# Kernel tuning notes

Measured on AMD Instinct MI355X. Metric: run time of the kernel, lower is better.

Reference implementation:

```python
import jax, jax.numpy as jnp
import numpy as np


def setup_inputs() -> dict:
    key = jax.random.key(0)
    ks = jax.random.split(key, 8)
    N, NL, C, E, P3, P2, P1 = 2048, 16, 128, 10, 23, 4, 1
    return {
        "x": jax.random.normal(ks[0], (N, NL, C), dtype=jnp.float32),
        "atom_types": jax.random.randint(ks[1], (N,), 0, E),
        "U3": jax.random.normal(ks[2], (NL, NL, NL, P3), dtype=jnp.float32),
        "U2": jax.random.normal(ks[3], (NL, NL, P2), dtype=jnp.float32),
        "U1": jax.random.normal(ks[4], (NL, P1), dtype=jnp.float32),
        "W3": jax.random.normal(ks[5], (E, P3, C), dtype=jnp.float32),
        "W2": jax.random.normal(ks[6], (E, P2, C), dtype=jnp.float32),
        "W1": jax.random.normal(ks[7], (E, P1, C), dtype=jnp.float32),
    }


def reference(x, atom_types, U3, U2, U1, W3, W2, W1):
    # MACE symmetric contraction, correlation order 3, per-atom-type weights.
    # x: [N, nl, C]; atom_types: [N]; U3: [nl,nl,nl,P3]; W3: [E,P3,C]; etc.
    w3 = W3[atom_types]  # [N, P3, C]
    w2 = W2[atom_types]  # [N, P2, C]
    w1 = W1[atom_types]  # [N, P1, C]
    # Correlation-3 term: c3[n,a,b,c] = sum_{i,k} U3[a,b,i,k] * w3[n,k,c] * x[n,i,c]
    xw = jnp.einsum('nkc,nic->nkic', w3, x)        # [N, P3, nl, C]
    c3 = jnp.einsum('abik,nkic->nabc', U3, xw)     # [N, nl, nl, C]
    # Add correlation-2 term, contract one nl index with x.
    c2 = c3 + jnp.einsum('abk,nkc->nabc', U2, w2)  # [N, nl, nl, C]
    c1 = jnp.einsum('nabc,nbc->nac', c2, x)        # [N, nl, C]
    # Add correlation-1 term, contract last nl index with x.
    c1 = c1 + jnp.einsum('ak,nkc->nac', U1, w1)    # [N, nl, C]
    out = jnp.einsum('nac,nac->nc', c1, x)         # [N, C]
    return out
```

## Files before the change

kernel.cpp:

```cpp
#include <hip/hip_runtime.h>


constexpr int NL = 16;
constexpr int CC = 128;
constexpr int EE = 10;
constexpr int P3 = 23;
constexpr int P2 = 4;
constexpr int NTRI = 816;
constexpr int NPAIR = 136;
constexpr int GG = 2;

constexpr int pairsBefore(int a) {
    int s = 0;
    for (int x = 0; x < a; x++) s += NL - x;
    return s;
}
constexpr int trisBefore(int a) {
    int s = 0;
    for (int x = 0; x < a; x++) s += (NL - x) * (NL - x + 1) / 2;
    return s;
}
static_assert(trisBefore(2) % 4 == 0 && trisBefore(4) % 4 == 0 && trisBefore(8) % 4 == 0, "");

__global__ void k_symU(const float* __restrict__ U3, const float* __restrict__ U2,
                       float* __restrict__ U3s, float* __restrict__ U2s,
                       float* __restrict__ out, int out_n, int* __restrict__ counts) {
    int gtid = blockIdx.x * blockDim.x + threadIdx.x;
    int nthreads = gridDim.x * blockDim.x;
    if (gtid < 16) counts[gtid] = 0;
    for (int idx = gtid; idx < out_n; idx += nthreads) out[idx] = 0.f;
    int idx = gtid;
    if (idx < NTRI * P3) {
        int tri = idx / P3, k = idx % P3;
        int rem = tri, a = 0;
        while (rem >= (NL - a) * (NL - a + 1) / 2) { rem -= (NL - a) * (NL - a + 1) / 2; a++; }
        int b = a;
        while (rem >= NL - b) { rem -= NL - b; b++; }
        int i = b + rem;
        auto u = [&](int p, int q, int r) { return U3[((p * NL + q) * NL + r) * P3 + k]; };
        float s = u(a,b,i) + u(a,i,b) + u(b,a,i) + u(b,i,a) + u(i,a,b) + u(i,b,a);
        int m = (a == b && b == i) ? 6 : ((a == b || b == i) ? 2 : 1);
        U3s[idx] = s / (float)m;
    } else if (idx < NTRI * P3 + NPAIR * P2) {
        int j = idx - NTRI * P3;
        int pr = j / P2, k = j % P2;
        int rem = pr, a = 0;
        while (rem >= NL - a) { rem -= NL - a; a++; }
        int b = a + rem;
        float s = U2[(a * NL + b) * P2 + k];
        if (a != b) s += U2[(b * NL + a) * P2 + k];
        U2s[pr * P2 + k] = s;
    }
}

__global__ __launch_bounds__(256) void k_buildA(const float* __restrict__ U3s,
                                                const float* __restrict__ U2s,
                                                const float* __restrict__ U1,
                                                const float* __restrict__ W3,
                                                const float* __restrict__ W2,
                                                const float* __restrict__ W1,
                                                float* __restrict__ A3, float* __restrict__ A2,
                                                float* __restrict__ A1) {
    int blk = blockIdx.x;
    int tid = threadIdx.x;
    if (blk < EE * 8) {
        int t = blk / 8, chunk = blk % 8;
        __shared__ float W3s[P3 * CC];
        __shared__ float U3c[102 * P3];
        for (int idx = tid; idx < P3 * CC; idx += 256) W3s[idx] = W3[t * P3 * CC + idx];
        for (int idx = tid; idx < 102 * P3; idx += 256) U3c[idx] = U3s[chunk * 102 * P3 + idx];
        __syncthreads();
        int c = tid & 127, h = tid >> 7;
        for (int j = 0; j < 51; j++) {
            int tsub = h * 51 + j;
            int tri = chunk * 102 + tsub;
            float s = 0.f;
            #pragma unroll
            for (int k = 0; k < P3; k++) s += U3c[tsub * P3 + k] * W3s[k * CC + c];
            A3[(((size_t)t * (NTRI / 4) + (tri >> 2)) * CC + c) * 4 + (tri & 3)] = s;
        }
    } else {
        int t = blk - EE * 8;
        __shared__ float W2s[P2 * CC];
        __shared__ float U2c[NPAIR * P2];
        for (int idx = tid; idx < P2 * CC; idx += 256) W2s[idx] = W2[t * P2 * CC + idx];
        for (int idx = tid; idx < NPAIR * P2; idx += 256) U2c[idx] = U2s[idx];
        __syncthreads();
        int c = tid & 127, h = tid >> 7;
        for (int j = 0; j < NPAIR / 2; j++) {
            int pr = h * (NPAIR / 2) + j;
            float s = 0.f;
            #pragma unroll
            for (int k = 0; k < P2; k++) s += U2c[pr * P2 + k] * W2s[k * CC + c];
            A2[((size_t)t * NPAIR + pr) * CC + c] = s;
        }
        if (h == 0)
            for (int a = 0; a < NL; a++)
                A1[((size_t)t * NL + a) * CC + c] = U1[a] * W1[t * CC + c];
    }
}

__global__ void k_bucket(const int* __restrict__ types, int* counts, int* buckets, int N) {
    int n = blockIdx.x * blockDim.x + threadIdx.x;
    if (n < N) {
        int t = types[n];
        int pos = atomicAdd(&counts[t], 1);
        buckets[t * N + pos] = n;
    }
}

__global__ void k_groups(const int* __restrict__ counts, const int* __restrict__ buckets,
                         int* __restrict__ groups, int* __restrict__ ngroups, int N) {
    __shared__ int goff[EE + 1];
    if (threadIdx.x == 0) {
        int off = 0;
        for (int t = 0; t < EE; t++) { goff[t] = off; off += (counts[t] + GG - 1) / GG; }
        goff[EE] = off;
        *ngroups = off;
    }
    __syncthreads();
    for (int t = 0; t < EE; t++) {
        int cnt = counts[t];
        int ng = (cnt + GG - 1) / GG;
        for (int g = threadIdx.x; g < ng; g += blockDim.x) {
            int* gr = &groups[(goff[t] + g) * 4];
            int nv = cnt - g * GG; if (nv > GG) nv = GG;
            gr[0] = t;
            gr[3] = nv;
            for (int j = 0; j < GG; j++) {
                int jj = j < nv ? j : nv - 1;
                gr[1 + j] = buckets[t * N + g * GG + jj];
            }
        }
    }
}

template <int A0, int A1v, bool LIN>
__device__ __forceinline__ void run_split(const float* __restrict__ x,
                                          const float4* __restrict__ a3v,
                                          const float* __restrict__ a2p,
                                          const float* __restrict__ a1p,
                                          const int (&na)[GG], int c, float (&acc)[GG]) {
    float xv[GG][NL];
    constexpr int L0 = LIN ? 0 : A0;
    #pragma unroll
    for (int g = 0; g < GG; g++)
        #pragma unroll
        for (int i = L0; i < NL; i++)
            xv[g][i] = x[((size_t)na[g] * NL + i) * CC + c];

    if (LIN) {
        #pragma unroll
        for (int a = 0; a < NL; a++) {
            float w = a1p[a * CC];
            #pragma unroll
            for (int g = 0; g < GG; g++) acc[g] += w * xv[g][a];
        }
    }

    float4 w4 = {0.f, 0.f, 0.f, 0.f};
    int tri = trisBefore(A0), pr = pairsBefore(A0);
    #pragma unroll
    for (int a = A0; a < A1v; a++) {
        float s[GG];
        #pragma unroll
        for (int g = 0; g < GG; g++) s[g] = 0.f;
        #pragma unroll
        for (int b = a; b < NL; b++) {
            float w2 = a2p[(size_t)pr * CC]; pr++;
            float r[GG];
            #pragma unroll
            for (int g = 0; g < GG; g++) r[g] = w2;
            #pragma unroll
            for (int i = b; i < NL; i++) {
                if ((tri & 3) == 0) w4 = a3v[(size_t)(tri >> 2) * CC];
                int rr = tri & 3;
                float w3 = (rr == 0) ? w4.x : (rr == 1) ? w4.y : (rr == 2) ? w4.z : w4.w;
                tri++;
                #pragma unroll
                for (int g = 0; g < GG; g++) r[g] += w3 * xv[g][i];
            }
            #pragma unroll
            for (int g = 0; g < GG; g++) s[g] += xv[g][b] * r[g];
        }
        #pragma unroll
        for (int g = 0; g < GG; g++) acc[g] += xv[g][a] * s[g];
    }
}

__global__ __launch_bounds__(CC) void k_main(const float* __restrict__ x,
                                             const float* __restrict__ A3,
                                             const float* __restrict__ A2,
                                             const float* __restrict__ A1,
                                             const int* __restrict__ groups,
                                             const int* __restrict__ ngroups,
                                             float* __restrict__ out) {
    int gidx = blockIdx.x;
    if (gidx >= *ngroups) return;
    const int* gr = groups + gidx * 4;
    int t = gr[0];
    int nvalid = gr[3];
    int c = threadIdx.x;

    int na[GG];
    #pragma unroll
    for (int g = 0; g < GG; g++) na[g] = gr[1 + g];

    const float4* a3v = (const float4*)A3 + (size_t)t * (NTRI / 4) * CC + c;
    const float* a2p = A2 + (size_t)t * NPAIR * CC + c;
    const float* a1p = A1 + (size_t)t * NL * CC + c;

    float acc[GG] = {0.f, 0.f};
    switch (blockIdx.y) {
        case 0: run_split<0, 2, true >(x, a3v, a2p, a1p, na, c, acc); break;
        case 1: run_split<2, 4, false>(x, a3v, a2p, a1p, na, c, acc); break;
        case 2: run_split<4, 8, false>(x, a3v, a2p, a1p, na, c, acc); break;
        default: run_split<8, 16, false>(x, a3v, a2p, a1p, na, c, acc); break;
    }

    #pragma unroll
    for (int g = 0; g < GG; g++)
        if (g < nvalid) atomicAdd(&out[(size_t)na[g] * CC + c], acc[g]);
}

extern "C" void kernel_launch(void* const* d_in, const int* in_sizes, int n_in,
                              void* d_out, int out_size, void* d_ws, size_t ws_size,
                              hipStream_t stream) {
    const float* x   = (const float*)d_in[0];
    const int* types = (const int*)d_in[1];
    const float* U3  = (const float*)d_in[2];
    const float* U2  = (const float*)d_in[3];
    const float* U1  = (const float*)d_in[4];
    const float* W3  = (const float*)d_in[5];
    const float* W2  = (const float*)d_in[6];
    const float* W1  = (const float*)d_in[7];
    float* out = (float*)d_out;
    int N = in_sizes[1];

    int ngmax = (N + GG - 1) / GG + EE;

    float* ws   = (float*)d_ws;
    float* U3s  = ws;
    float* U2s  = U3s + NTRI * P3;
    float* A3   = U2s + NPAIR * P2;
    float* A2   = A3 + (size_t)EE * NTRI * CC;
    float* A1   = A2 + (size_t)EE * NPAIR * CC;
    int* counts  = (int*)(A1 + (size_t)EE * NL * CC);
    int* buckets = counts + 16;
    int* groups  = buckets + (size_t)EE * N;
    int* ngroups = groups + (size_t)ngmax * 4;

    hipLaunchKernelGGL(k_symU, dim3(76), dim3(256), 0, stream,
                       U3, U2, U3s, U2s, out, out_size, counts);
    hipLaunchKernelGGL(k_buildA, dim3(EE * 8 + EE), dim3(256), 0, stream,
                       U3s, U2s, U1, W3, W2, W1, A3, A2, A1);
    hipLaunchKernelGGL(k_bucket, dim3((N + 255) / 256), dim3(256), 0, stream,
                       types, counts, buckets, N);
    hipLaunchKernelGGL(k_groups, dim3(1), dim3(256), 0, stream,
                       counts, buckets, groups, ngroups, N);
    hipLaunchKernelGGL(k_main, dim3(ngmax, 4), dim3(CC), 0, stream,
                       x, A3, A2, A1, groups, ngroups, out);
}
```

Baseline: 132.3 us.

## Fuse U symmetrization into A-build, drop group kernel, process four atoms per block

Folds U3/U2 symmetrization, zeroing of the output and resetting of counts into the A-table build kernel. It also removes the separate group-building kernel, so k_main now finds its atom type and atom indices directly from counts and buckets. The atoms per block (GG) go from 2 to 4, so each loaded A3 coefficient is reused across more atoms. Together this cuts two kernel launches and their serialization. The trade is redundant symmetrization work in every block, more registers for x values in k_main, and a per-block scan over the type counts.

```diff
diff --git a/kernel.cpp b/kernel.cpp
--- a/kernel.cpp
+++ b/kernel.cpp
@@ -8,7 +8,7 @@
 constexpr int P2 = 4;
 constexpr int NTRI = 816;
 constexpr int NPAIR = 136;
-constexpr int GG = 2;
+constexpr int GG = 4;
 
 constexpr int pairsBefore(int a) {
     int s = 0;
@@ -22,45 +22,24 @@
 }
 static_assert(trisBefore(2) % 4 == 0 && trisBefore(4) % 4 == 0 && trisBefore(8) % 4 == 0, "");
 
-__global__ void k_symU(const float* __restrict__ U3, const float* __restrict__ U2,
-                       float* __restrict__ U3s, float* __restrict__ U2s,
-                       float* __restrict__ out, int out_n, int* __restrict__ counts) {
-    int gtid = blockIdx.x * blockDim.x + threadIdx.x;
-    int nthreads = gridDim.x * blockDim.x;
-    if (gtid < 16) counts[gtid] = 0;
-    for (int idx = gtid; idx < out_n; idx += nthreads) out[idx] = 0.f;
-    int idx = gtid;
-    if (idx < NTRI * P3) {
-        int tri = idx / P3, k = idx % P3;
-        int rem = tri, a = 0;
-        while (rem >= (NL - a) * (NL - a + 1) / 2) { rem -= (NL - a) * (NL - a + 1) / 2; a++; }
-        int b = a;
-        while (rem >= NL - b) { rem -= NL - b; b++; }
-        int i = b + rem;
-        auto u = [&](int p, int q, int r) { return U3[((p * NL + q) * NL + r) * P3 + k]; };
-        float s = u(a,b,i) + u(a,i,b) + u(b,a,i) + u(b,i,a) + u(i,a,b) + u(i,b,a);
-        int m = (a == b && b == i) ? 6 : ((a == b || b == i) ? 2 : 1);
-        U3s[idx] = s / (float)m;
-    } else if (idx < NTRI * P3 + NPAIR * P2) {
-        int j = idx - NTRI * P3;
-        int pr = j / P2, k = j % P2;
-        int rem = pr, a = 0;
-        while (rem >= NL - a) { rem -= NL - a; a++; }
-        int b = a + rem;
-        float s = U2[(a * NL + b) * P2 + k];
-        if (a != b) s += U2[(b * NL + a) * P2 + k];
-        U2s[pr * P2 + k] = s;
-    }
-}
-
-__global__ __launch_bounds__(256) void k_buildA(const float* __restrict__ U3s,
-                                                const float* __restrict__ U2s,
-                                                const float* __restrict__ U1,
-                                                const float* __restrict__ W3,
-                                                const float* __restrict__ W2,
-                                                const float* __restrict__ W1,
-                                                float* __restrict__ A3, float* __restrict__ A2,
-                                                float* __restrict__ A1) {
+__device__ __forceinline__ void unrankTri(int tri, int& a, int& b, int& i) {
+    int rem = tri; a = 0;
+    while (rem >= (NL - a) * (NL - a + 1) / 2) { rem -= (NL - a) * (NL - a + 1) / 2; a++; }
+    b = a;
+    while (rem >= NL - b) { rem -= NL - b; b++; }
+    i = b + rem;
+}
+
+__global__ __launch_bounds__(256) void k_prep(const float* __restrict__ U3,
+                                              const float* __restrict__ U2,
+                                              const float* __restrict__ U1,
+                                              const float* __restrict__ W3,
+                                              const float* __restrict__ W2,
+                                              const float* __restrict__ W1,
+                                              float* __restrict__ A3, float* __restrict__ A2,
+                                              float* __restrict__ A1,
+                                              float* __restrict__ out, int out_n,
+                                              int* __restrict__ counts) {
     int blk = blockIdx.x;
     int tid = threadIdx.x;
     if (blk < EE * 8) {
@@ -68,7 +47,15 @@
         __shared__ float W3s[P3 * CC];
         __shared__ float U3c[102 * P3];
         for (int idx = tid; idx < P3 * CC; idx += 256) W3s[idx] = W3[t * P3 * CC + idx];
-        for (int idx = tid; idx < 102 * P3; idx += 256) U3c[idx] = U3s[chunk * 102 * P3 + idx];
+        for (int idx = tid; idx < 102 * P3; idx += 256) {
+            int tsub = idx / P3, k = idx - tsub * P3;
+            int a, b, i;
+            unrankTri(chunk * 102 + tsub, a, b, i);
+            auto u = [&](int p, int q, int r) { return U3[((p * NL + q) * NL + r) * P3 + k]; };
+            float s = u(a,b,i) + u(a,i,b) + u(b,a,i) + u(b,i,a) + u(i,a,b) + u(i,b,a);
+            int m = (a == b && b == i) ? 6 : ((a == b || b == i) ? 2 : 1);
+            U3c[idx] = s / (float)m;
+        }
         __syncthreads();
         int c = tid & 127, h = tid >> 7;
         for (int j = 0; j < 51; j++) {
@@ -84,7 +71,17 @@
         __shared__ float W2s[P2 * CC];
         __shared__ float U2c[NPAIR * P2];
         for (int idx = tid; idx < P2 * CC; idx += 256) W2s[idx] = W2[t * P2 * CC + idx];
-        for (int idx = tid; idx < NPAIR * P2; idx += 256) U2c[idx] = U2s[idx];
+        for (int idx = tid; idx < NPAIR * P2; idx += 256) {
+            int pr = idx >> 2, k = idx & 3;
+            int rem = pr, a = 0;
+            while (rem >= NL - a) { rem -= NL - a; a++; }
+            int b = a + rem;
+            float s = U2[(a * NL + b) * P2 + k];
+            if (a != b) s += U2[(b * NL + a) * P2 + k];
+            U2c[idx] = s;
+        }
+        for (int i = t * 256 + tid; i < out_n; i += EE * 256) out[i] = 0.f;
+        if (t == 0 && tid < 16) counts[tid] = 0;
         __syncthreads();
         int c = tid & 127, h = tid >> 7;
         for (int j = 0; j < NPAIR / 2; j++) {
@@ -106,32 +103,6 @@
         int t = types[n];
         int pos = atomicAdd(&counts[t], 1);
         buckets[t * N + pos] = n;
-    }
-}
-
-__global__ void k_groups(const int* __restrict__ counts, const int* __restrict__ buckets,
-                         int* __restrict__ groups, int* __restrict__ ngroups, int N) {
-    __shared__ int goff[EE + 1];
-    if (threadIdx.x == 0) {
-        int off = 0;
-        for (int t = 0; t < EE; t++) { goff[t] = off; off += (counts[t] + GG - 1) / GG; }
-        goff[EE] = off;
-        *ngroups = off;
-    }
-    __syncthreads();
-    for (int t = 0; t < EE; t++) {
-        int cnt = counts[t];
-        int ng = (cnt + GG - 1) / GG;
-        for (int g = threadIdx.x; g < ng; g += blockDim.x) {
-            int* gr = &groups[(goff[t] + g) * 4];
-            int nv = cnt - g * GG; if (nv > GG) nv = GG;
-            gr[0] = t;
-            gr[3] = nv;
-            for (int j = 0; j < GG; j++) {
-                int jj = j < nv ? j : nv - 1;
-                gr[1 + j] = buckets[t * N + g * GG + jj];
-            }
-        }
     }
 }
 
@@ -192,25 +163,35 @@
                                              const float* __restrict__ A3,
                                              const float* __restrict__ A2,
                                              const float* __restrict__ A1,
-                                             const int* __restrict__ groups,
-                                             const int* __restrict__ ngroups,
+                                             const int* __restrict__ counts,
+                                             const int* __restrict__ buckets,
+                                             int N,
                                              float* __restrict__ out) {
     int gidx = blockIdx.x;
-    if (gidx >= *ngroups) return;
-    const int* gr = groups + gidx * 4;
-    int t = gr[0];
-    int nvalid = gr[3];
+    int t = -1, slot = 0, cnt = 0, base = 0;
+    #pragma unroll
+    for (int tt = 0; tt < EE; tt++) {
+        int ctt = counts[tt];
+        int ng = (ctt + GG - 1) >> 2;
+        if (t < 0 && gidx < base + ng) { t = tt; slot = gidx - base; cnt = ctt; }
+        base += ng;
+    }
+    if (t < 0) return;
+
     int c = threadIdx.x;
-
+    int nvalid = cnt - slot * GG; if (nvalid > GG) nvalid = GG;
     int na[GG];
     #pragma unroll
-    for (int g = 0; g < GG; g++) na[g] = gr[1 + g];
+    for (int g = 0; g < GG; g++) {
+        int j = slot * GG + g; if (j > cnt - 1) j = cnt - 1;
+        na[g] = buckets[t * N + j];
+    }
 
     const float4* a3v = (const float4*)A3 + (size_t)t * (NTRI / 4) * CC + c;
     const float* a2p = A2 + (size_t)t * NPAIR * CC + c;
     const float* a1p = A1 + (size_t)t * NL * CC + c;
 
-    float acc[GG] = {0.f, 0.f};
+    float acc[GG] = {0.f, 0.f, 0.f, 0.f};
     switch (blockIdx.y) {
         case 0: run_split<0, 2, true >(x, a3v, a2p, a1p, na, c, acc); break;
         case 1: run_split<2, 4, false>(x, a3v, a2p, a1p, na, c, acc); break;
@@ -240,24 +221,16 @@
     int ngmax = (N + GG - 1) / GG + EE;
 
     float* ws   = (float*)d_ws;
-    float* U3s  = ws;
-    float* U2s  = U3s + NTRI * P3;
-    float* A3   = U2s + NPAIR * P2;
+    float* A3   = ws;
     float* A2   = A3 + (size_t)EE * NTRI * CC;
     float* A1   = A2 + (size_t)EE * NPAIR * CC;
     int* counts  = (int*)(A1 + (size_t)EE * NL * CC);
     int* buckets = counts + 16;
-    int* groups  = buckets + (size_t)EE * N;
-    int* ngroups = groups + (size_t)ngmax * 4;
-
-    hipLaunchKernelGGL(k_symU, dim3(76), dim3(256), 0, stream,
-                       U3, U2, U3s, U2s, out, out_size, counts);
-    hipLaunchKernelGGL(k_buildA, dim3(EE * 8 + EE), dim3(256), 0, stream,
-                       U3s, U2s, U1, W3, W2, W1, A3, A2, A1);
+
+    hipLaunchKernelGGL(k_prep, dim3(EE * 8 + EE), dim3(256), 0, stream,
+                       U3, U2, U1, W3, W2, W1, A3, A2, A1, out, out_size, counts);
     hipLaunchKernelGGL(k_bucket, dim3((N + 255) / 256), dim3(256), 0, stream,
                        types, counts, buckets, N);
-    hipLaunchKernelGGL(k_groups, dim3(1), dim3(256), 0, stream,
-                       counts, buckets, groups, ngroups, N);
     hipLaunchKernelGGL(k_main, dim3(ngmax, 4), dim3(CC), 0, stream,
-                       x, A3, A2, A1, groups, ngroups, out);
-}
+                       x, A3, A2, A1, counts, buckets, N, out);
+}
```

After: 139.5 us. +5.4%, slower.
